# Kernel optimization log

Measured on AMD Instinct MI355X. Metric: run time of the kernel, lower is better.

Reference implementation:

```python
import jax, jax.numpy as jnp
import numpy as np

B, L, DIM = 4, 2048, 1024
EXPAND, D_STATE, D_CONV = 2, 16, 4
D_INNER = EXPAND * DIM          # 2048
DT_RANK = DIM // 16             # 64
MLP_HID = 4 * DIM


def setup_inputs() -> dict:
    key = jax.random.key(0)
    ks = jax.random.split(key, 20)
    s = 0.02
    inp = {
        "hidden_states": jax.random.normal(ks[0], (B, L, DIM), jnp.float32),
        "cond": jax.random.normal(ks[1], (B, DIM), jnp.float32),
        # norm (LayerNorm with affine)
        "norm_w": jnp.ones((DIM,), jnp.float32),
        "norm_b": jnp.zeros((DIM,), jnp.float32),
        # adaLN: Linear(dim, 6*dim)
        "ada_w": jax.random.normal(ks[2], (6 * DIM, DIM), jnp.float32) * s,
        "ada_b": jnp.zeros((6 * DIM,), jnp.float32),
        # Mamba mixer params
        "in_proj_w": jax.random.normal(ks[3], (2 * D_INNER, DIM), jnp.float32) * s,
        "conv_w": jax.random.normal(ks[4], (D_INNER, 1, D_CONV), jnp.float32) * s,
        "conv_b": jnp.zeros((D_INNER,), jnp.float32),
        "x_proj_w": jax.random.normal(ks[5], (DT_RANK + 2 * D_STATE, D_INNER), jnp.float32) * s,
        "dt_proj_w": jax.random.normal(ks[6], (D_INNER, DT_RANK), jnp.float32) * s,
        "dt_proj_b": jax.random.uniform(ks[7], (D_INNER,), jnp.float32, -4.0, -2.0),
        "A_log": jnp.log(jnp.broadcast_to(jnp.arange(1, D_STATE + 1, dtype=jnp.float32), (D_INNER, D_STATE))),
        "Dp": jnp.ones((D_INNER,), jnp.float32),
        "out_proj_w": jax.random.normal(ks[8], (DIM, D_INNER), jnp.float32) * s,
        # MLP
        "fc1_w": jax.random.normal(ks[9], (MLP_HID, DIM), jnp.float32) * s,
        "fc1_b": jnp.zeros((MLP_HID,), jnp.float32),
        "fc2_w": jax.random.normal(ks[10], (DIM, MLP_HID), jnp.float32) * s,
        "fc2_b": jnp.zeros((DIM,), jnp.float32),
    }
    return inp


def _layernorm(x, w, b, eps):
    mu = jnp.mean(x, axis=-1, keepdims=True)
    var = jnp.mean(jnp.square(x - mu), axis=-1, keepdims=True)
    y = (x - mu) * jax.lax.rsqrt(var + eps)
    return y * w + b if w is not None else y


def _modulate(x, shift, scale):
    # x: [B,L,D]; shift/scale: [B,D]
    return x * (1.0 + scale[:, None, :]) + shift[:, None, :]


def _mamba(x_in, in_proj_w, conv_w, conv_b, x_proj_w, dt_proj_w, dt_proj_b, A_log, Dp, out_proj_w):
    # x_in: [B,L,DIM]
    xz = jnp.einsum("bld,ed->ble", x_in, in_proj_w)        # [B,L,2*Di]
    x, z = jnp.split(xz, 2, axis=-1)                        # each [B,L,Di]
    # causal depthwise conv over L
    x_ncl = jnp.transpose(x, (0, 2, 1))                     # [B,Di,L]
    x_ncl = jax.lax.conv_general_dilated(
        x_ncl, conv_w, window_strides=(1,), padding=[(D_CONV - 1, 0)],
        feature_group_count=D_INNER, dimension_numbers=("NCH", "OIH", "NCH"))
    x = jnp.transpose(x_ncl, (0, 2, 1)) + conv_b            # [B,L,Di]
    x = jax.nn.silu(x)
    x_dbl = jnp.einsum("bld,ed->ble", x, x_proj_w)          # [B,L,dt_rank+2*N]
    dt, Bm, Cm = jnp.split(x_dbl, [DT_RANK, DT_RANK + D_STATE], axis=-1)
    dt = jax.nn.softplus(jnp.einsum("blr,dr->bld", dt, dt_proj_w) + dt_proj_b)  # [B,L,Di]
    A = -jnp.exp(A_log)                                     # [Di,N]

    def step(h, inps):
        dt_t, B_t, C_t, x_t = inps                          # [B,Di],[B,N],[B,N],[B,Di]
        dA = jnp.exp(dt_t[..., None] * A)                   # [B,Di,N]
        dBx = (dt_t * x_t)[..., None] * B_t[:, None, :]     # [B,Di,N]
        h = h * dA + dBx
        y = jnp.einsum("bdn,bn->bd", h, C_t)
        return h, y

    h0 = jnp.zeros((x.shape[0], D_INNER, D_STATE), x.dtype)
    xs = (jnp.transpose(dt, (1, 0, 2)), jnp.transpose(Bm, (1, 0, 2)),
          jnp.transpose(Cm, (1, 0, 2)), jnp.transpose(x, (1, 0, 2)))
    _, ys = jax.lax.scan(step, h0, xs)                      # [L,B,Di]
    y = jnp.transpose(ys, (1, 0, 2)) + x * Dp               # [B,L,Di]
    y = y * jax.nn.silu(z)
    return jnp.einsum("bld,od->blo", y, out_proj_w)         # [B,L,DIM]


def reference(hidden_states, cond, norm_w, norm_b, ada_w, ada_b, in_proj_w, conv_w,
              conv_b, x_proj_w, dt_proj_w, dt_proj_b, A_log, Dp, out_proj_w,
              fc1_w, fc1_b, fc2_w, fc2_b):
    residual = hidden_states                                # residual=None path
    hs = _layernorm(residual, norm_w, norm_b, 1e-5)
    mods = jax.nn.silu(cond) @ ada_w.T + ada_b              # [B,6*DIM]
    shift_msa, scale_msa, gate_msa, shift_mlp, scale_mlp, gate_mlp = jnp.split(mods, 6, axis=1)
    hs = gate_msa[:, None, :] * _mamba(_modulate(hs, shift_msa, scale_msa),
                                       in_proj_w, conv_w, conv_b, x_proj_w,
                                       dt_proj_w, dt_proj_b, A_log, Dp, out_proj_w)
    h2 = _modulate(_layernorm(hs, None, None, 1e-6), shift_mlp, scale_mlp)
    h2 = jax.nn.gelu(h2 @ fc1_w.T + fc1_b, approximate=True) @ fc2_w.T + fc2_b
    hs = hs + gate_mlp[:, None, :] * h2
    return (hs, residual)
```

## Files before the change

### kernel.cpp

```cpp
#include <hip/hip_runtime.h>
#include <hip/hip_bf16.h>


typedef unsigned short ushort_t;
typedef __attribute__((ext_vector_type(8))) short short8;
typedef __attribute__((ext_vector_type(4))) float floatx4;
typedef __attribute__((ext_vector_type(4))) unsigned short ushort4v;

#define DEVI __device__ __forceinline__

DEVI float b2f(ushort_t u) { union { unsigned int i; float f; } v; v.i = ((unsigned int)u) << 16; return v.f; }
DEVI ushort_t f2b(float f) {
    union { float f; unsigned int i; } v; v.f = f;
    unsigned int r = v.i + 0x7fffu + ((v.i >> 16) & 1u);
    return (ushort_t)(r >> 16);
}
DEVI float sigmoidf_(float x) { return 1.f / (1.f + __expf(-x)); }
DEVI float siluf_(float x) { return x * sigmoidf_(x); }
DEVI float softplusf_(float x) { return (x > 20.f) ? x : log1pf(__expf(x)); }
DEVI float gelu_tanh_(float x) {
    float c = 0.7978845608028654f * (x + 0.044715f * x * x * x);
    return 0.5f * x * (1.f + tanhf(c));
}
DEVI void async16(ushort_t* lds, const ushort_t* g) {
    __builtin_amdgcn_global_load_lds((const __attribute__((address_space(1))) void*)g,
                                     (__attribute__((address_space(3))) void*)lds,
                                     16, 0, 0);
}

DEVI void remap_tile(int bid, int Mt, int Nt, int& mt, int& nt) {
    const int nwg = Mt * Nt;
    const int cpx = nwg >> 3;
    const int v = (bid & 7) * cpx + (bid >> 3);
    if (((Mt & 7) == 0) && ((Nt & 7) == 0)) {
        const int s = v >> 6, w = v & 63;
        const int smt = s % (Mt >> 3), snt = s / (Mt >> 3);
        mt = smt * 8 + (w >> 3);
        nt = snt * 8 + (w & 7);
    } else {
        mt = v % Mt;
        nt = v / Mt;
    }
}

__global__ void detect_kernel(const void* norm_w, int* flag) {
    if (threadIdx.x == 0)
        flag[0] = (((const unsigned int*)norm_w)[0] == 0x3F800000u) ? 1 : 0;
}

__global__ __launch_bounds__(256) void convert_w_kernel(
    const void* __restrict__ src, ushort_t* __restrict__ dst, int n8,
    const int* __restrict__ flag)
{
    int i = blockIdx.x * 256 + threadIdx.x;
    if (i >= n8) return;
    if (*flag) {
        const float4* s = (const float4*)src;
        float4 a = s[2 * i], b = s[2 * i + 1];
        short8 o;
        o[0] = (short)f2b(a.x); o[1] = (short)f2b(a.y);
        o[2] = (short)f2b(a.z); o[3] = (short)f2b(a.w);
        o[4] = (short)f2b(b.x); o[5] = (short)f2b(b.y);
        o[6] = (short)f2b(b.z); o[7] = (short)f2b(b.w);
        ((short8*)dst)[i] = o;
    } else {
        ((short8*)dst)[i] = ((const short8*)src)[i];
    }
}

__global__ __launch_bounds__(256) void canon_bias_kernel(
    const void* __restrict__ src, float* __restrict__ dst, int n,
    const int* __restrict__ flag)
{
    int i = blockIdx.x * 256 + threadIdx.x;
    if (i >= n) return;
    dst[i] = (*flag) ? ((const float*)src)[i] : b2f(((const ushort_t*)src)[i]);
}

__global__ __launch_bounds__(256) void residual_kernel(
    const void* __restrict__ src, void* __restrict__ dst, const int* __restrict__ flag)
{
    size_t i = (size_t)blockIdx.x * 256 + threadIdx.x;
    if (*flag) {
        ((float4*)((float*)dst + 8388608))[i] = ((const float4*)src)[i];
    } else {
        ((ushort4v*)((ushort_t*)dst + 8388608))[i] = ((const ushort4v*)src)[i];
    }
}

__global__ __launch_bounds__(256) void ada_kernel(
    const void* __restrict__ condv, const void* __restrict__ ada_wv,
    const void* __restrict__ ada_bv, float* __restrict__ mods,
    const int* __restrict__ flag)
{
    __shared__ float sc[4096];
    const int tid = threadIdx.x;
    const bool f32 = (*flag != 0);
    if (f32) {
        const float* cf = (const float*)condv;
        for (int i = tid; i < 4096; i += 256) sc[i] = siluf_(cf[i]);
    } else {
        const ushort_t* cb = (const ushort_t*)condv;
        for (int i = tid; i < 4096; i += 256) sc[i] = siluf_(b2f(cb[i]));
    }
    __syncthreads();
    const int j = blockIdx.x * 256 + tid;
    float bb = f32 ? ((const float*)ada_bv)[j] : b2f(((const ushort_t*)ada_bv)[j]);
    float s0 = bb, s1 = bb, s2 = bb, s3 = bb;
    if (f32) {
        const float4* w4 = ((const float4*)ada_wv) + (size_t)j * 256;
        for (int d4 = 0; d4 < 256; d4++) {
            float4 w = w4[d4];
            float wv[4] = {w.x, w.y, w.z, w.w};
#pragma unroll
            for (int e = 0; e < 4; e++) {
                int d = d4 * 4 + e;
                s0 += sc[d] * wv[e];
                s1 += sc[1024 + d] * wv[e];
                s2 += sc[2048 + d] * wv[e];
                s3 += sc[3072 + d] * wv[e];
            }
        }
    } else {
        const ushort_t* wrow = ((const ushort_t*)ada_wv) + (size_t)j * 1024;
        for (int d = 0; d < 1024; d += 8) {
            short8 w8 = *(const short8*)(wrow + d);
#pragma unroll
            for (int e = 0; e < 8; e++) {
                float wv = b2f(((const ushort_t*)&w8)[e]);
                s0 += sc[d + e] * wv;
                s1 += sc[1024 + d + e] * wv;
                s2 += sc[2048 + d + e] * wv;
                s3 += sc[3072 + d + e] * wv;
            }
        }
    }
    mods[0 * 6144 + j] = s0;
    mods[1 * 6144 + j] = s1;
    mods[2 * 6144 + j] = s2;
    mods[3 * 6144 + j] = s3;
}

__global__ __launch_bounds__(256) void ln1_mod_kernel(
    const void* __restrict__ hiddenv, const void* __restrict__ nwv,
    const void* __restrict__ nbv, const float* __restrict__ mods,
    ushort_t* __restrict__ xout, const int* __restrict__ flag)
{
    const int t = blockIdx.x, tid = threadIdx.x;
    const int bb = t >> 11;
    const bool f32 = (*flag != 0);
    float vv[4], s = 0.f, ss = 0.f;
    if (f32) {
        float4 u = ((const float4*)((const float*)hiddenv + (size_t)t * 1024))[tid];
        vv[0] = u.x; vv[1] = u.y; vv[2] = u.z; vv[3] = u.w;
    } else {
        ushort4v u = ((const ushort4v*)((const ushort_t*)hiddenv + (size_t)t * 1024))[tid];
#pragma unroll
        for (int j = 0; j < 4; j++) vv[j] = b2f(u[j]);
    }
#pragma unroll
    for (int j = 0; j < 4; j++) { s += vv[j]; ss += vv[j] * vv[j]; }
#pragma unroll
    for (int off = 32; off > 0; off >>= 1) { s += __shfl_down(s, off); ss += __shfl_down(ss, off); }
    __shared__ float red[8];
    const int wave = tid >> 6, lane = tid & 63;
    if (lane == 0) { red[wave] = s; red[4 + wave] = ss; }
    __syncthreads();
    s = red[0] + red[1] + red[2] + red[3];
    ss = red[4] + red[5] + red[6] + red[7];
    const float mu = s * (1.f / 1024.f);
    const float var = ss * (1.f / 1024.f) - mu * mu;
    const float rstd = rsqrtf(var + 1e-5f);
    const float* mrow = mods + (size_t)bb * 6144;
    ushort4v o;
#pragma unroll
    for (int j = 0; j < 4; j++) {
        int d = tid * 4 + j;
        float w = f32 ? ((const float*)nwv)[d] : b2f(((const ushort_t*)nwv)[d]);
        float b = f32 ? ((const float*)nbv)[d] : b2f(((const ushort_t*)nbv)[d]);
        float y = (vv[j] - mu) * rstd * w + b;
        y = y * (1.f + mrow[1024 + d]) + mrow[d];
        o[j] = f2b(y);
    }
    ((ushort4v*)(xout + (size_t)t * 1024))[tid] = o;
}

__global__ __launch_bounds__(256) void ln2_mod_kernel(
    const ushort_t* __restrict__ hs, const float* __restrict__ mods,
    ushort_t* __restrict__ xout)
{
    const int t = blockIdx.x, tid = threadIdx.x;
    const int bb = t >> 11;
    ushort4v u = ((const ushort4v*)(hs + (size_t)t * 1024))[tid];
    float vv[4], s = 0.f, ss = 0.f;
#pragma unroll
    for (int j = 0; j < 4; j++) { vv[j] = b2f(u[j]); s += vv[j]; ss += vv[j] * vv[j]; }
#pragma unroll
    for (int off = 32; off > 0; off >>= 1) { s += __shfl_down(s, off); ss += __shfl_down(ss, off); }
    __shared__ float red[8];
    const int wave = tid >> 6, lane = tid & 63;
    if (lane == 0) { red[wave] = s; red[4 + wave] = ss; }
    __syncthreads();
    s = red[0] + red[1] + red[2] + red[3];
    ss = red[4] + red[5] + red[6] + red[7];
    const float mu = s * (1.f / 1024.f);
    const float var = ss * (1.f / 1024.f) - mu * mu;
    const float rstd = rsqrtf(var + 1e-6f);
    const float* mrow = mods + (size_t)bb * 6144;
    ushort4v o;
#pragma unroll
    for (int j = 0; j < 4; j++) {
        int d = tid * 4 + j;
        float y = (vv[j] - mu) * rstd;
        y = y * (1.f + mrow[4096 + d]) + mrow[3072 + d];
        o[j] = f2b(y);
    }
    ((ushort4v*)(xout + (size_t)t * 1024))[tid] = o;
}

__global__ __launch_bounds__(256) void conv_silu_kernel(
    const ushort_t* __restrict__ xb, const void* __restrict__ cwv,
    const void* __restrict__ cbv, ushort_t* __restrict__ xc,
    const int* __restrict__ flag)
{
    const int t = blockIdx.x;
    const int l = t & 2047;
    const int c0 = threadIdx.x * 8;
    const bool f32 = (*flag != 0);
    float acc[8];
    float wlf[32];
    if (f32) {
        const float* cbf = (const float*)cbv;
#pragma unroll
        for (int j = 0; j < 8; j++) acc[j] = cbf[c0 + j];
        const float4* cw4 = (const float4*)((const float*)cwv + (size_t)c0 * 4);
#pragma unroll
        for (int q = 0; q < 8; q++) {
            float4 w = cw4[q];
            wlf[q * 4 + 0] = w.x; wlf[q * 4 + 1] = w.y;
            wlf[q * 4 + 2] = w.z; wlf[q * 4 + 3] = w.w;
        }
    } else {
        const ushort_t* cbb = (const ushort_t*)cbv;
#pragma unroll
        for (int j = 0; j < 8; j++) acc[j] = b2f(cbb[c0 + j]);
        const ushort_t* cwb = (const ushort_t*)cwv + (size_t)c0 * 4;
#pragma unroll
        for (int q = 0; q < 32; q++) wlf[q] = b2f(cwb[q]);
    }
#pragma unroll
    for (int k = 0; k < 4; k++) {
        int tl = l + k - 3;
        if (tl < 0) continue;
        short8 xv = *(const short8*)(xb + (size_t)(t + k - 3) * 2048 + c0);
#pragma unroll
        for (int j = 0; j < 8; j++)
            acc[j] += b2f(((const ushort_t*)&xv)[j]) * wlf[j * 4 + k];
    }
    short8 o;
#pragma unroll
    for (int j = 0; j < 8; j++) ((ushort_t*)&o)[j] = f2b(siluf_(acc[j]));
    *(short8*)(xc + (size_t)t * 2048 + c0) = o;
}

__global__ __launch_bounds__(256) void scan_phase1(
    const ushort_t* __restrict__ dtb, const ushort_t* __restrict__ xcv,
    const ushort_t* __restrict__ xdbl, const void* __restrict__ A_logv,
    ushort_t* __restrict__ Hloc, ushort_t* __restrict__ Pst,
    const int* __restrict__ flag)
{
    const int blk = blockIdx.x;
    const int dblk = blk & 7;
    const int c = (blk >> 3) & 31;
    const int b = blk >> 8;
    const int d = dblk * 256 + threadIdx.x;
    const bool f32 = (*flag != 0);
    float Av[16];
#pragma unroll
    for (int n = 0; n < 16; n++) {
        float al = f32 ? ((const float*)A_logv)[(size_t)d * 16 + n]
                       : b2f(((const ushort_t*)A_logv)[(size_t)d * 16 + n]);
        Av[n] = -__expf(al);
    }
    float h[16], Pa[16];
#pragma unroll
    for (int n = 0; n < 16; n++) { h[n] = 0.f; Pa[n] = 1.f; }
    const int t0 = c * 64;
    size_t tb = ((size_t)b * 2048 + t0) * 2048 + d;
    float dtv = b2f(dtb[tb]);
    float xv  = b2f(xcv[tb]);
    for (int tt = 0; tt < 64; ++tt) {
        float dtn = b2f(dtb[tb + 2048]);
        float xn  = b2f(xcv[tb + 2048]);
        const ushort_t* bp = xdbl + ((size_t)b * 2048 + t0 + tt) * 96 + 64;
        short8 B8a = *(const short8*)bp;
        short8 B8b = *(const short8*)(bp + 8);
        float dtx = dtv * xv;
#pragma unroll
        for (int n = 0; n < 8; n++) {
            float dA = __expf(dtv * Av[n]);
            h[n] = h[n] * dA + dtx * b2f(((const ushort_t*)&B8a)[n]);
            Pa[n] *= dA;
        }
#pragma unroll
        for (int n = 8; n < 16; n++) {
            float dA = __expf(dtv * Av[n]);
            h[n] = h[n] * dA + dtx * b2f(((const ushort_t*)&B8b)[n - 8]);
            Pa[n] *= dA;
        }
        dtv = dtn; xv = xn; tb += 2048;
    }
    const size_t o = (((size_t)c * 4 + b) * 16) * 2048 + d;
#pragma unroll
    for (int n = 0; n < 16; n++) {
        Hloc[o + (size_t)n * 2048] = f2b(h[n]);
        Pst [o + (size_t)n * 2048] = f2b(Pa[n]);
    }
}

__global__ __launch_bounds__(256) void scan_phase2(
    const ushort_t* __restrict__ Hloc, const ushort_t* __restrict__ Pst,
    float* __restrict__ Hin)
{
    const int gi = blockIdx.x * 256 + threadIdx.x;
    const int d = gi & 2047;
    const int n = (gi >> 11) & 15;
    const int b = gi >> 15;
    float h = 0.f;
    const size_t o0 = ((size_t)b * 16 + n) * 2048 + d;
    for (int c = 0; c < 32; ++c) {
        const size_t o = o0 + (size_t)c * (4 * 16 * 2048);
        Hin[o] = h;
        h = b2f(Hloc[o]) + b2f(Pst[o]) * h;
    }
}

__global__ __launch_bounds__(256) void scan_phase3(
    const ushort_t* __restrict__ dtb, ushort_t* __restrict__ xc,
    const ushort_t* __restrict__ xdbl, const ushort_t* __restrict__ zbuf,
    const void* __restrict__ A_logv, const void* __restrict__ Dpv,
    const float* __restrict__ Hin, const int* __restrict__ flag)
{
    const int blk = blockIdx.x;
    const int dblk = blk & 7;
    const int c = (blk >> 3) & 31;
    const int b = blk >> 8;
    const int d = dblk * 256 + threadIdx.x;
    const bool f32 = (*flag != 0);
    float Av[16];
#pragma unroll
    for (int n = 0; n < 16; n++) {
        float al = f32 ? ((const float*)A_logv)[(size_t)d * 16 + n]
                       : b2f(((const ushort_t*)A_logv)[(size_t)d * 16 + n]);
        Av[n] = -__expf(al);
    }
    const float Dv = f32 ? ((const float*)Dpv)[d] : b2f(((const ushort_t*)Dpv)[d]);
    float h[16];
    {
        const size_t o = (((size_t)c * 4 + b) * 16) * 2048 + d;
#pragma unroll
        for (int n = 0; n < 16; n++) h[n] = Hin[o + (size_t)n * 2048];
    }
    const int t0 = c * 64;
    size_t tb = ((size_t)b * 2048 + t0) * 2048 + d;
    float dtv = b2f(dtb[tb]);
    float xv  = b2f(xc[tb]);
    float zv  = b2f(zbuf[tb]);
    for (int tt = 0; tt < 64; ++tt) {
        float dtn = b2f(dtb[tb + 2048]);
        float xn  = b2f(xc[tb + 2048]);
        float zn  = b2f(zbuf[tb + 2048]);
        const ushort_t* bp = xdbl + ((size_t)b * 2048 + t0 + tt) * 96 + 64;
        short8 B8a = *(const short8*)bp;
        short8 B8b = *(const short8*)(bp + 8);
        short8 C8a = *(const short8*)(bp + 16);
        short8 C8b = *(const short8*)(bp + 24);
        float dtx = dtv * xv;
        float y = 0.f;
#pragma unroll
        for (int n = 0; n < 8; n++) {
            float dA = __expf(dtv * Av[n]);
            h[n] = h[n] * dA + dtx * b2f(((const ushort_t*)&B8a)[n]);
            y += h[n] * b2f(((const ushort_t*)&C8a)[n]);
        }
#pragma unroll
        for (int n = 8; n < 16; n++) {
            float dA = __expf(dtv * Av[n]);
            h[n] = h[n] * dA + dtx * b2f(((const ushort_t*)&B8b)[n - 8]);
            y += h[n] * b2f(((const ushort_t*)&C8b)[n - 8]);
        }
        float yo = (y + xv * Dv) * siluf_(zv);
        xc[tb] = f2b(yo);
        dtv = dtn; xv = xn; zv = zn; tb += 2048;
    }
}

template <int EPI>
DEVI void epi_store(int row, int col, float v,
                    void* C0, void* C1, int ldc,
                    const float* bias, const float* mods,
                    const ushort_t* hs, int fl)
{
    if constexpr (EPI == 0) {
        if (col < 2048)
            ((ushort_t*)C0)[(size_t)row * 2048 + col] = f2b(v);
        else
            ((ushort_t*)C1)[(size_t)row * 2048 + (col - 2048)] = f2b(v);
    } else if constexpr (EPI == 1) {
        ((ushort_t*)C0)[(size_t)row * ldc + col] = f2b(v);
    } else if constexpr (EPI == 2) {
        v += bias[col];
        ((ushort_t*)C0)[(size_t)row * ldc + col] = f2b(softplusf_(v));
    } else if constexpr (EPI == 3) {
        const int bb = row >> 11;
        v *= mods[(size_t)bb * 6144 + 2048 + col];
        ((ushort_t*)C0)[(size_t)row * ldc + col] = f2b(v);
    } else if constexpr (EPI == 4) {
        v += bias[col];
        ((ushort_t*)C0)[(size_t)row * ldc + col] = f2b(gelu_tanh_(v));
    } else if constexpr (EPI == 5) {
        v += bias[col];
        const int bb = row >> 11;
        float o = b2f(hs[(size_t)row * 1024 + col]) + mods[(size_t)bb * 6144 + 5120 + col] * v;
        if (fl)
            ((float*)C0)[(size_t)row * ldc + col] = o;
        else
            ((ushort_t*)C0)[(size_t)row * ldc + col] = f2b(o);
    }
}

#define KLOOP_PIPE(NT)                                               \
    stage(0, 0);                                                     \
    {                                                                \
        int cur = 0;                                                 \
        for (int kt = 0; kt < (NT); kt++) {                          \
            if (kt + 1 < (NT)) {                                     \
                stage(cur ^ 1, kt + 1);                              \
                asm volatile("s_waitcnt vmcnt(8)" ::: "memory");     \
            } else {                                                 \
                asm volatile("s_waitcnt vmcnt(0)" ::: "memory");     \
            }                                                        \
            __builtin_amdgcn_sched_barrier(0);                       \
            __builtin_amdgcn_s_barrier();                            \
            __builtin_amdgcn_sched_barrier(0);                       \
            __builtin_amdgcn_s_setprio(1);                           \
            compute(cur);                                            \
            __builtin_amdgcn_s_setprio(0);                           \
            __builtin_amdgcn_sched_barrier(0);                       \
            __builtin_amdgcn_s_barrier();                            \
            __builtin_amdgcn_sched_barrier(0);                       \
            cur ^= 1;                                                \
        }                                                            \
    }

template <int EPI>
__global__ __launch_bounds__(256) void gemm_bt(
    const ushort_t* __restrict__ A, int lda,
    const ushort_t* __restrict__ W,
    int M, int N, int K,
    void* __restrict__ C0, void* __restrict__ C1, int ldc,
    const float* __restrict__ bias,
    const float* __restrict__ mods,
    const ushort_t* __restrict__ hs,
    const int* __restrict__ flag)
{
    __shared__ __align__(16) ushort_t sA[2][128 * 64];
    __shared__ __align__(16) ushort_t sB[2][128 * 64];
    const int tid = threadIdx.x;
    const int wave = tid >> 6, lane = tid & 63;
    int mt, nt;
    remap_tile(blockIdx.x, M >> 7, (N + 127) >> 7, mt, nt);
    const int m0 = mt << 7, n0 = nt << 7;
    const int wr = wave >> 1, wc = wave & 1;
    const int r = tid >> 3, c8 = tid & 7;
    const int rs7 = r & 7;
    int fl = 0;
    if constexpr (EPI == 5) fl = *flag;

    floatx4 acc[4][4];
#pragma unroll
    for (int m = 0; m < 4; m++)
#pragma unroll
        for (int nn = 0; nn < 4; nn++) acc[m][nn] = floatx4{0.f, 0.f, 0.f, 0.f};

    auto stage = [&](int buf, int kt) {
        const int kb = kt << 6;
#pragma unroll
        for (int i = 0; i < 4; i++) {
            const int row = i * 32 + r;
            async16(&sA[buf][(size_t)row * 64 + c8 * 8],
                    A + (size_t)(m0 + row) * lda + kb + ((c8 ^ rs7) << 3));
            int rB = n0 + row; if (rB >= N) rB = N - 1;
            async16(&sB[buf][(size_t)row * 64 + c8 * 8],
                    W + (size_t)rB * K + kb + ((c8 ^ rs7) << 3));
        }
    };
    auto compute = [&](int buf) {
#pragma unroll
        for (int kk = 0; kk < 2; kk++) {
            const int sw = ((kk * 4 + (lane >> 4)) ^ (lane & 7)) << 3;
            short8 bfr[4];
#pragma unroll
            for (int nn = 0; nn < 4; nn++)
                bfr[nn] = *(const short8*)&sB[buf][(size_t)(wc * 64 + nn * 16 + (lane & 15)) * 64 + sw];
#pragma unroll
            for (int m = 0; m < 4; m++) {
                short8 af = *(const short8*)&sA[buf][(size_t)(wr * 64 + m * 16 + (lane & 15)) * 64 + sw];
#pragma unroll
                for (int nn = 0; nn < 4; nn++)
                    acc[m][nn] = __builtin_amdgcn_mfma_f32_16x16x32_bf16(af, bfr[nn], acc[m][nn], 0, 0, 0);
            }
        }
    };

    const int NT = K >> 6;
    KLOOP_PIPE(NT)

    const int erow = wr * 64 + ((lane >> 4) << 2);
    const int ecol = wc * 64 + (lane & 15);
#pragma unroll
    for (int m = 0; m < 4; m++)
#pragma unroll
        for (int nn = 0; nn < 4; nn++) {
            const int col = n0 + ecol + nn * 16;
            if (col >= N) continue;
#pragma unroll
            for (int rr = 0; rr < 4; rr++)
                epi_store<EPI>(m0 + erow + m * 16 + rr, col, acc[m][nn][rr],
                               C0, C1, ldc, bias, mods, hs, fl);
        }
}

template <int EPI>
__global__ __launch_bounds__(512) void gemm256(
    const ushort_t* __restrict__ A, int lda,
    const ushort_t* __restrict__ W,
    int M, int N, int K,
    void* __restrict__ C0, void* __restrict__ C1, int ldc,
    const float* __restrict__ bias,
    const float* __restrict__ mods,
    const ushort_t* __restrict__ hs,
    const int* __restrict__ flag)
{
    __shared__ __align__(16) ushort_t sA[2][256 * 64];
    __shared__ __align__(16) ushort_t sB[2][256 * 64];
    const int tid = threadIdx.x;
    const int wave = tid >> 6, lane = tid & 63;
    int mt, nt;
    remap_tile(blockIdx.x, M >> 8, N >> 8, mt, nt);
    const int m0 = mt << 8, n0 = nt << 8;
    const int wr = wave >> 2, wc = wave & 3;
    const int r = tid >> 3, c8 = tid & 7;
    const int rs7 = r & 7;
    int fl = 0;
    if constexpr (EPI == 5) fl = *flag;

    floatx4 acc[8][4];
#pragma unroll
    for (int m = 0; m < 8; m++)
#pragma unroll
        for (int nn = 0; nn < 4; nn++) acc[m][nn] = floatx4{0.f, 0.f, 0.f, 0.f};

    auto stage = [&](int buf, int kt) {
        const int kb = kt << 6;
#pragma unroll
        for (int i = 0; i < 4; i++) {
            const int row = i * 64 + r;
            async16(&sA[buf][(size_t)row * 64 + c8 * 8],
                    A + (size_t)(m0 + row) * lda + kb + ((c8 ^ rs7) << 3));
            async16(&sB[buf][(size_t)row * 64 + c8 * 8],
                    W + (size_t)(n0 + row) * K + kb + ((c8 ^ rs7) << 3));
        }
    };
    auto compute = [&](int buf) {
#pragma unroll
        for (int kk = 0; kk < 2; kk++) {
            const int sw = ((kk * 4 + (lane >> 4)) ^ (lane & 7)) << 3;
            short8 bfr[4];
#pragma unroll
            for (int nn = 0; nn < 4; nn++)
                bfr[nn] = *(const short8*)&sB[buf][(size_t)(wc * 64 + nn * 16 + (lane & 15)) * 64 + sw];
#pragma unroll
            for (int m = 0; m < 8; m++) {
                short8 af = *(const short8*)&sA[buf][(size_t)(wr * 128 + m * 16 + (lane & 15)) * 64 + sw];
#pragma unroll
                for (int nn = 0; nn < 4; nn++)
                    acc[m][nn] = __builtin_amdgcn_mfma_f32_16x16x32_bf16(af, bfr[nn], acc[m][nn], 0, 0, 0);
            }
        }
    };

    const int NT = K >> 6;
    KLOOP_PIPE(NT)

    const int erow = wr * 128 + ((lane >> 4) << 2);
    const int ecol = wc * 64 + (lane & 15);
#pragma unroll
    for (int m = 0; m < 8; m++)
#pragma unroll
        for (int nn = 0; nn < 4; nn++) {
            const int col = n0 + ecol + nn * 16;
            if (col >= N) continue;
#pragma unroll
            for (int rr = 0; rr < 4; rr++)
                epi_store<EPI>(m0 + erow + m * 16 + rr, col, acc[m][nn][rr],
                               C0, C1, ldc, bias, mods, hs, fl);
        }
}

extern "C" void kernel_launch(void* const* d_in, const int* in_sizes, int n_in,
                              void* d_out, int out_size, void* d_ws, size_t ws_size,
                              hipStream_t stream)
{
    const void* hidden   = d_in[0];
    const void* cond     = d_in[1];
    const void* norm_w   = d_in[2];
    const void* norm_b   = d_in[3];
    const void* ada_w    = d_in[4];
    const void* ada_b    = d_in[5];
    const void* in_proj  = d_in[6];
    const void* conv_w   = d_in[7];
    const void* conv_b   = d_in[8];
    const void* x_proj   = d_in[9];
    const void* dt_w     = d_in[10];
    const void* dt_b     = d_in[11];
    const void* A_log    = d_in[12];
    const void* Dp       = d_in[13];
    const void* out_proj = d_in[14];
    const void* fc1_w    = d_in[15];
    const void* fc1_b    = d_in[16];
    const void* fc2_w    = d_in[17];
    const void* fc2_b    = d_in[18];

    constexpr size_t OFF_FLAG  = 0;
    constexpr size_t OFF_MODS  = 256;
    constexpr size_t OFF_DTB_F = 131072;
    constexpr size_t OFF_FC1B  = 139264;
    constexpr size_t OFF_FC2B  = 155648;
    constexpr size_t OFF_WIN   = 262144;
    constexpr size_t OFF_WXP   = 8650752;
    constexpr size_t OFF_WDT   = 9043968;
    constexpr size_t OFF_WOUT  = 9306112;
    constexpr size_t OFF_WFC1  = 13500416;
    constexpr size_t OFF_WFC2  = 21889024;
    constexpr size_t OFF_XBUF  = 30277632;
    constexpr size_t OFF_ZBUF  = 63832064;
    constexpr size_t OFF_XCONV = 97386496;
    constexpr size_t OFF_XIN   = 130940928;
    constexpr size_t OFF_XDBL  = 147718144;
    constexpr size_t OFF_HS    = 149291008;
    constexpr size_t WS_NEED   = 166068224;
    if (ws_size < WS_NEED) return;

    char* ws = (char*)d_ws;
    int*      flag   = (int*)(ws + OFF_FLAG);
    float*    mods   = (float*)(ws + OFF_MODS);
    float*    dtb_f  = (float*)(ws + OFF_DTB_F);
    float*    fc1b_f = (float*)(ws + OFF_FC1B);
    float*    fc2b_f = (float*)(ws + OFF_FC2B);
    ushort_t* w_in   = (ushort_t*)(ws + OFF_WIN);
    ushort_t* w_xp   = (ushort_t*)(ws + OFF_WXP);
    ushort_t* w_dt   = (ushort_t*)(ws + OFF_WDT);
    ushort_t* w_out  = (ushort_t*)(ws + OFF_WOUT);
    ushort_t* w_fc1  = (ushort_t*)(ws + OFF_WFC1);
    ushort_t* w_fc2  = (ushort_t*)(ws + OFF_WFC2);
    ushort_t* xbuf   = (ushort_t*)(ws + OFF_XBUF);
    ushort_t* zbuf   = (ushort_t*)(ws + OFF_ZBUF);
    ushort_t* x_conv = (ushort_t*)(ws + OFF_XCONV);
    ushort_t* x_in   = (ushort_t*)(ws + OFF_XIN);
    ushort_t* x_dbl  = (ushort_t*)(ws + OFF_XDBL);
    ushort_t* hsb    = (ushort_t*)(ws + OFF_HS);
    ushort_t* dtb    = xbuf;
    ushort_t* h1     = xbuf;
    ushort_t* h2in   = x_in;
    ushort_t* Hloc   = (ushort_t*)(ws + OFF_XIN);
    ushort_t* Pst    = (ushort_t*)(ws + OFF_XIN + 8388608);
    float*    Hin    = (float*)(ws + OFF_HS);

    detect_kernel<<<1, 64, 0, stream>>>(norm_w, flag);

    convert_w_kernel<<<2048, 256, 0, stream>>>(in_proj, w_in, 524288, flag);
    convert_w_kernel<<<96, 256, 0, stream>>>(x_proj, w_xp, 24576, flag);
    convert_w_kernel<<<64, 256, 0, stream>>>(dt_w, w_dt, 16384, flag);
    convert_w_kernel<<<1024, 256, 0, stream>>>(out_proj, w_out, 262144, flag);
    convert_w_kernel<<<2048, 256, 0, stream>>>(fc1_w, w_fc1, 524288, flag);
    convert_w_kernel<<<2048, 256, 0, stream>>>(fc2_w, w_fc2, 524288, flag);
    canon_bias_kernel<<<8, 256, 0, stream>>>(dt_b, dtb_f, 2048, flag);
    canon_bias_kernel<<<16, 256, 0, stream>>>(fc1_b, fc1b_f, 4096, flag);
    canon_bias_kernel<<<4, 256, 0, stream>>>(fc2_b, fc2b_f, 1024, flag);

    residual_kernel<<<8192, 256, 0, stream>>>(hidden, d_out, flag);

    ada_kernel<<<24, 256, 0, stream>>>(cond, ada_w, ada_b, mods, flag);
    ln1_mod_kernel<<<8192, 256, 0, stream>>>(hidden, norm_w, norm_b, mods, x_in, flag);
    gemm256<0><<<32 * 16, 512, 0, stream>>>(x_in, 1024, w_in, 8192, 4096, 1024,
                                            xbuf, zbuf, 2048, nullptr, nullptr, nullptr, flag);
    conv_silu_kernel<<<8192, 256, 0, stream>>>(xbuf, conv_w, conv_b, x_conv, flag);
    gemm_bt<1><<<64 * 1, 256, 0, stream>>>(x_conv, 2048, w_xp, 8192, 96, 2048,
                                           x_dbl, nullptr, 96, nullptr, nullptr, nullptr, flag);
    gemm_bt<2><<<64 * 16, 256, 0, stream>>>(x_dbl, 96, w_dt, 8192, 2048, 64,
                                            dtb, nullptr, 2048, dtb_f, nullptr, nullptr, flag);
    scan_phase1<<<1024, 256, 0, stream>>>(dtb, x_conv, x_dbl, A_log, Hloc, Pst, flag);
    scan_phase2<<<512, 256, 0, stream>>>(Hloc, Pst, Hin);
    scan_phase3<<<1024, 256, 0, stream>>>(dtb, x_conv, x_dbl, zbuf, A_log, Dp, Hin, flag);
    gemm_bt<3><<<64 * 8, 256, 0, stream>>>(x_conv, 2048, w_out, 8192, 1024, 2048,
                                           hsb, nullptr, 1024, nullptr, mods, nullptr, flag);
    ln2_mod_kernel<<<8192, 256, 0, stream>>>(hsb, mods, h2in);
    gemm256<4><<<32 * 16, 512, 0, stream>>>(h2in, 1024, w_fc1, 8192, 4096, 1024,
                                            h1, nullptr, 4096, fc1b_f, nullptr, nullptr, flag);
    gemm_bt<5><<<64 * 8, 256, 0, stream>>>(h1, 4096, w_fc2, 8192, 1024, 4096,
                                           d_out, nullptr, 1024, fc2b_f, mods, hsb, flag);
}
```

Before: 775.6 us.

## Merge prep kernels, split-K x_proj GEMM, phase-pipelined 256 GEMM with finer LDS staging

All weight and bias conversions now run in one launch, and the dtype flag is computed inline from norm_w, so the detect kernel is gone. The residual copy is folded into the first layernorm kernel. The skinny x_proj GEMM (N=96) becomes a 4-way split-K into fp32 partials followed by a reduce kernel, raising its block count from 64 to 256. The 256-tile GEMM is restructured into four K-phases per tile with barriers, prefetch interleaved per phase, setprio around the MFMAs and a new LDS layout. This adds more barriers per K step and an extra partial-sum pass through memory.

New measurement: 757.0 us. -2.4%, faster.

```diff
diff --git a/kernel.cpp b/kernel.cpp
--- a/kernel.cpp
+++ b/kernel.cpp
@@ -15,6 +15,7 @@
     unsigned int r = v.i + 0x7fffu + ((v.i >> 16) & 1u);
     return (ushort_t)(r >> 16);
 }
+DEVI bool is_f32(const void* nw) { return ((const unsigned int*)nw)[0] == 0x3F800000u; }
 DEVI float sigmoidf_(float x) { return 1.f / (1.f + __expf(-x)); }
 DEVI float siluf_(float x) { return x * sigmoidf_(x); }
 DEVI float softplusf_(float x) { return (x > 20.f) ? x : log1pf(__expf(x)); }
@@ -43,59 +44,61 @@
     }
 }
 
-__global__ void detect_kernel(const void* norm_w, int* flag) {
-    if (threadIdx.x == 0)
-        flag[0] = (((const unsigned int*)norm_w)[0] == 0x3F800000u) ? 1 : 0;
-}
-
-__global__ __launch_bounds__(256) void convert_w_kernel(
-    const void* __restrict__ src, ushort_t* __restrict__ dst, int n8,
-    const int* __restrict__ flag)
-{
-    int i = blockIdx.x * 256 + threadIdx.x;
+__global__ __launch_bounds__(256) void convert_all_kernel(
+    const void* __restrict__ in_proj, const void* __restrict__ x_proj,
+    const void* __restrict__ dt_w, const void* __restrict__ out_proj,
+    const void* __restrict__ fc1_w, const void* __restrict__ fc2_w,
+    const void* __restrict__ dt_b, const void* __restrict__ fc1_b,
+    const void* __restrict__ fc2_b,
+    ushort_t* __restrict__ w_in, ushort_t* __restrict__ w_xp,
+    ushort_t* __restrict__ w_dt, ushort_t* __restrict__ w_out,
+    ushort_t* __restrict__ w_fc1, ushort_t* __restrict__ w_fc2,
+    float* __restrict__ dtb_f, float* __restrict__ fc1b_f,
+    float* __restrict__ fc2b_f, const void* __restrict__ nw)
+{
+    const bool f32 = is_f32(nw);
+    int b = blockIdx.x;
+    const void* src; ushort_t* dst; int n8;
+    if (b < 2048)      { src = in_proj;  dst = w_in;  n8 = 524288; }
+    else if (b < 2144) { src = x_proj;   dst = w_xp;  n8 = 24576;  b -= 2048; }
+    else if (b < 2208) { src = dt_w;     dst = w_dt;  n8 = 16384;  b -= 2144; }
+    else if (b < 3232) { src = out_proj; dst = w_out; n8 = 262144; b -= 2208; }
+    else if (b < 5280) { src = fc1_w;    dst = w_fc1; n8 = 524288; b -= 3232; }
+    else if (b < 7328) { src = fc2_w;    dst = w_fc2; n8 = 524288; b -= 5280; }
+    else {
+        b -= 7328;
+        const void* bs; float* bd; int n;
+        if (b < 8)       { bs = dt_b;  bd = dtb_f;  n = 2048; }
+        else if (b < 24) { bs = fc1_b; bd = fc1b_f; n = 4096; b -= 8; }
+        else             { bs = fc2_b; bd = fc2b_f; n = 1024; b -= 24; }
+        int i = b * 256 + threadIdx.x;
+        if (i < n) bd[i] = f32 ? ((const float*)bs)[i] : b2f(((const ushort_t*)bs)[i]);
+        return;
+    }
+    int i = b * 256 + threadIdx.x;
     if (i >= n8) return;
-    if (*flag) {
+    if (f32) {
         const float4* s = (const float4*)src;
-        float4 a = s[2 * i], b = s[2 * i + 1];
+        float4 a = s[2 * i], c = s[2 * i + 1];
         short8 o;
         o[0] = (short)f2b(a.x); o[1] = (short)f2b(a.y);
         o[2] = (short)f2b(a.z); o[3] = (short)f2b(a.w);
-        o[4] = (short)f2b(b.x); o[5] = (short)f2b(b.y);
-        o[6] = (short)f2b(b.z); o[7] = (short)f2b(b.w);
+        o[4] = (short)f2b(c.x); o[5] = (short)f2b(c.y);
+        o[6] = (short)f2b(c.z); o[7] = (short)f2b(c.w);
         ((short8*)dst)[i] = o;
     } else {
         ((short8*)dst)[i] = ((const short8*)src)[i];
     }
 }
 
-__global__ __launch_bounds__(256) void canon_bias_kernel(
-    const void* __restrict__ src, float* __restrict__ dst, int n,
-    const int* __restrict__ flag)
-{
-    int i = blockIdx.x * 256 + threadIdx.x;
-    if (i >= n) return;
-    dst[i] = (*flag) ? ((const float*)src)[i] : b2f(((const ushort_t*)src)[i]);
-}
-
-__global__ __launch_bounds__(256) void residual_kernel(
-    const void* __restrict__ src, void* __restrict__ dst, const int* __restrict__ flag)
-{
-    size_t i = (size_t)blockIdx.x * 256 + threadIdx.x;
-    if (*flag) {
-        ((float4*)((float*)dst + 8388608))[i] = ((const float4*)src)[i];
-    } else {
-        ((ushort4v*)((ushort_t*)dst + 8388608))[i] = ((const ushort4v*)src)[i];
-    }
-}
-
 __global__ __launch_bounds__(256) void ada_kernel(
     const void* __restrict__ condv, const void* __restrict__ ada_wv,
     const void* __restrict__ ada_bv, float* __restrict__ mods,
-    const int* __restrict__ flag)
+    const void* __restrict__ nw)
 {
     __shared__ float sc[4096];
     const int tid = threadIdx.x;
-    const bool f32 = (*flag != 0);
+    const bool f32 = is_f32(nw);
     if (f32) {
         const float* cf = (const float*)condv;
         for (int i = tid; i < 4096; i += 256) sc[i] = siluf_(cf[i]);
@@ -141,22 +144,24 @@
     mods[3 * 6144 + j] = s3;
 }
 
-__global__ __launch_bounds__(256) void ln1_mod_kernel(
+__global__ __launch_bounds__(256) void ln1_res_kernel(
     const void* __restrict__ hiddenv, const void* __restrict__ nwv,
     const void* __restrict__ nbv, const float* __restrict__ mods,
-    ushort_t* __restrict__ xout, const int* __restrict__ flag)
+    ushort_t* __restrict__ xout, void* __restrict__ dout)
 {
     const int t = blockIdx.x, tid = threadIdx.x;
     const int bb = t >> 11;
-    const bool f32 = (*flag != 0);
+    const bool f32 = is_f32(nwv);
     float vv[4], s = 0.f, ss = 0.f;
     if (f32) {
         float4 u = ((const float4*)((const float*)hiddenv + (size_t)t * 1024))[tid];
         vv[0] = u.x; vv[1] = u.y; vv[2] = u.z; vv[3] = u.w;
+        ((float4*)((float*)dout + 8388608))[(size_t)t * 256 + tid] = u;
     } else {
         ushort4v u = ((const ushort4v*)((const ushort_t*)hiddenv + (size_t)t * 1024))[tid];
 #pragma unroll
         for (int j = 0; j < 4; j++) vv[j] = b2f(u[j]);
+        ((ushort4v*)((ushort_t*)dout + 8388608))[(size_t)t * 256 + tid] = u;
     }
 #pragma unroll
     for (int j = 0; j < 4; j++) { s += vv[j]; ss += vv[j] * vv[j]; }
@@ -221,12 +226,12 @@
 __global__ __launch_bounds__(256) void conv_silu_kernel(
     const ushort_t* __restrict__ xb, const void* __restrict__ cwv,
     const void* __restrict__ cbv, ushort_t* __restrict__ xc,
-    const int* __restrict__ flag)
+    const void* __restrict__ nw)
 {
     const int t = blockIdx.x;
     const int l = t & 2047;
     const int c0 = threadIdx.x * 8;
-    const bool f32 = (*flag != 0);
+    const bool f32 = is_f32(nw);
     float acc[8];
     float wlf[32];
     if (f32) {
@@ -267,14 +272,14 @@
     const ushort_t* __restrict__ dtb, const ushort_t* __restrict__ xcv,
     const ushort_t* __restrict__ xdbl, const void* __restrict__ A_logv,
     ushort_t* __restrict__ Hloc, ushort_t* __restrict__ Pst,
-    const int* __restrict__ flag)
+    const void* __restrict__ nw)
 {
     const int blk = blockIdx.x;
     const int dblk = blk & 7;
     const int c = (blk >> 3) & 31;
     const int b = blk >> 8;
     const int d = dblk * 256 + threadIdx.x;
-    const bool f32 = (*flag != 0);
+    const bool f32 = is_f32(nw);
     float Av[16];
 #pragma unroll
     for (int n = 0; n < 16; n++) {
@@ -339,14 +344,14 @@
     const ushort_t* __restrict__ dtb, ushort_t* __restrict__ xc,
     const ushort_t* __restrict__ xdbl, const ushort_t* __restrict__ zbuf,
     const void* __restrict__ A_logv, const void* __restrict__ Dpv,
-    const float* __restrict__ Hin, const int* __restrict__ flag)
+    const float* __restrict__ Hin, const void* __restrict__ nw)
 {
     const int blk = blockIdx.x;
     const int dblk = blk & 7;
     const int c = (blk >> 3) & 31;
     const int b = blk >> 8;
     const int d = dblk * 256 + threadIdx.x;
-    const bool f32 = (*flag != 0);
+    const bool f32 = is_f32(nw);
     float Av[16];
 #pragma unroll
     for (int n = 0; n < 16; n++) {
@@ -426,6 +431,8 @@
             ((float*)C0)[(size_t)row * ldc + col] = o;
         else
             ((ushort_t*)C0)[(size_t)row * ldc + col] = f2b(o);
+    } else if constexpr (EPI == 6) {
+        ((float*)C0)[(size_t)row * ldc + col] = v;
     }
 }
 
@@ -456,26 +463,34 @@
 template <int EPI>
 __global__ __launch_bounds__(256) void gemm_bt(
     const ushort_t* __restrict__ A, int lda,
-    const ushort_t* __restrict__ W,
+    const ushort_t* __restrict__ W, int ldw,
     int M, int N, int K,
     void* __restrict__ C0, void* __restrict__ C1, int ldc,
     const float* __restrict__ bias,
     const float* __restrict__ mods,
     const ushort_t* __restrict__ hs,
-    const int* __restrict__ flag)
+    const void* __restrict__ nwp)
 {
     __shared__ __align__(16) ushort_t sA[2][128 * 64];
     __shared__ __align__(16) ushort_t sB[2][128 * 64];
     const int tid = threadIdx.x;
     const int wave = tid >> 6, lane = tid & 63;
     int mt, nt;
-    remap_tile(blockIdx.x, M >> 7, (N + 127) >> 7, mt, nt);
+    if constexpr (EPI == 6) {
+        mt = blockIdx.x & 63; nt = 0;
+        const int kc = blockIdx.x >> 6;
+        A += (size_t)kc * 512;
+        W += (size_t)kc * 512;
+        C0 = (float*)C0 + (size_t)kc * 8192 * 96;
+    } else {
+        remap_tile(blockIdx.x, M >> 7, (N + 127) >> 7, mt, nt);
+    }
     const int m0 = mt << 7, n0 = nt << 7;
     const int wr = wave >> 1, wc = wave & 1;
     const int r = tid >> 3, c8 = tid & 7;
     const int rs7 = r & 7;
     int fl = 0;
-    if constexpr (EPI == 5) fl = *flag;
+    if constexpr (EPI == 5) fl = is_f32(nwp) ? 1 : 0;
 
     floatx4 acc[4][4];
 #pragma unroll
@@ -492,7 +507,7 @@
                     A + (size_t)(m0 + row) * lda + kb + ((c8 ^ rs7) << 3));
             int rB = n0 + row; if (rB >= N) rB = N - 1;
             async16(&sB[buf][(size_t)row * 64 + c8 * 8],
-                    W + (size_t)rB * K + kb + ((c8 ^ rs7) << 3));
+                    W + (size_t)rB * ldw + kb + ((c8 ^ rs7) << 3));
         }
     };
     auto compute = [&](int buf) {
@@ -534,26 +549,27 @@
 template <int EPI>
 __global__ __launch_bounds__(512) void gemm256(
     const ushort_t* __restrict__ A, int lda,
-    const ushort_t* __restrict__ W,
+    const ushort_t* __restrict__ W, int ldw,
     int M, int N, int K,
     void* __restrict__ C0, void* __restrict__ C1, int ldc,
     const float* __restrict__ bias,
     const float* __restrict__ mods,
     const ushort_t* __restrict__ hs,
-    const int* __restrict__ flag)
-{
-    __shared__ __align__(16) ushort_t sA[2][256 * 64];
-    __shared__ __align__(16) ushort_t sB[2][256 * 64];
+    const void* __restrict__ nwp)
+{
+    __shared__ __align__(16) ushort_t sA[2][4][256 * 16];
+    __shared__ __align__(16) ushort_t sB[2][4][256 * 16];
     const int tid = threadIdx.x;
     const int wave = tid >> 6, lane = tid & 63;
+    const int l15 = lane & 15, j8 = lane >> 4;
     int mt, nt;
     remap_tile(blockIdx.x, M >> 8, N >> 8, mt, nt);
     const int m0 = mt << 8, n0 = nt << 8;
     const int wr = wave >> 2, wc = wave & 3;
-    const int r = tid >> 3, c8 = tid & 7;
-    const int rs7 = r & 7;
+    const int srow = tid >> 1, scs = tid & 1;
+    const int ssrc = scs ^ ((srow >> 2) & 1);
     int fl = 0;
-    if constexpr (EPI == 5) fl = *flag;
+    if constexpr (EPI == 5) fl = is_f32(nwp) ? 1 : 0;
 
     floatx4 acc[8][4];
 #pragma unroll
@@ -561,40 +577,67 @@
 #pragma unroll
         for (int nn = 0; nn < 4; nn++) acc[m][nn] = floatx4{0.f, 0.f, 0.f, 0.f};
 
-    auto stage = [&](int buf, int kt) {
-        const int kb = kt << 6;
-#pragma unroll
-        for (int i = 0; i < 4; i++) {
-            const int row = i * 64 + r;
-            async16(&sA[buf][(size_t)row * 64 + c8 * 8],
-                    A + (size_t)(m0 + row) * lda + kb + ((c8 ^ rs7) << 3));
-            async16(&sB[buf][(size_t)row * 64 + c8 * 8],
-                    W + (size_t)(n0 + row) * K + kb + ((c8 ^ rs7) << 3));
-        }
+    auto stage = [&](int buf, int kt, int p) {
+        const int kb = (kt << 6) + (p << 4);
+        async16(&sA[buf][p][srow * 16 + scs * 8],
+                A + (size_t)(m0 + srow) * lda + kb + ssrc * 8);
+        async16(&sB[buf][p][srow * 16 + scs * 8],
+                W + (size_t)(n0 + srow) * ldw + kb + ssrc * 8);
     };
-    auto compute = [&](int buf) {
-#pragma unroll
-        for (int kk = 0; kk < 2; kk++) {
-            const int sw = ((kk * 4 + (lane >> 4)) ^ (lane & 7)) << 3;
-            short8 bfr[4];
-#pragma unroll
-            for (int nn = 0; nn < 4; nn++)
-                bfr[nn] = *(const short8*)&sB[buf][(size_t)(wc * 64 + nn * 16 + (lane & 15)) * 64 + sw];
-#pragma unroll
-            for (int m = 0; m < 8; m++) {
-                short8 af = *(const short8*)&sA[buf][(size_t)(wr * 128 + m * 16 + (lane & 15)) * 64 + sw];
-#pragma unroll
-                for (int nn = 0; nn < 4; nn++)
-                    acc[m][nn] = __builtin_amdgcn_mfma_f32_16x16x32_bf16(af, bfr[nn], acc[m][nn], 0, 0, 0);
-            }
-        }
-    };
+
+#define G256_PHASE(P, MLO, KK)                                                  \
+    {                                                                           \
+        if (pre) {                                                              \
+            stage(cur ^ 1, kt + 1, P);                                          \
+            asm volatile("s_waitcnt vmcnt(4)" ::: "memory");                    \
+        } else if (P == 2) {                                                    \
+            asm volatile("s_waitcnt vmcnt(0)" ::: "memory");                    \
+        }                                                                       \
+        __builtin_amdgcn_sched_barrier(0);                                      \
+        __builtin_amdgcn_s_barrier();                                           \
+        __builtin_amdgcn_sched_barrier(0);                                      \
+        short8 bfr[4], af[4];                                                   \
+        _Pragma("unroll")                                                       \
+        for (int nn = 0; nn < 4; nn++) {                                        \
+            const int row = wc * 64 + nn * 16 + l15;                            \
+            bfr[nn] = *(const short8*)&sB[cur][(KK) * 2 + (j8 >> 1)]            \
+                          [row * 16 + (((j8 & 1) ^ ((row >> 2) & 1)) << 3)];    \
+        }                                                                       \
+        _Pragma("unroll")                                                       \
+        for (int i = 0; i < 4; i++) {                                           \
+            const int row = wr * 128 + ((MLO) + i) * 16 + l15;                  \
+            af[i] = *(const short8*)&sA[cur][(KK) * 2 + (j8 >> 1)]              \
+                        [row * 16 + (((j8 & 1) ^ ((row >> 2) & 1)) << 3)];      \
+        }                                                                       \
+        __builtin_amdgcn_s_setprio(1);                                          \
+        _Pragma("unroll")                                                       \
+        for (int i = 0; i < 4; i++)                                             \
+            _Pragma("unroll")                                                   \
+            for (int nn = 0; nn < 4; nn++)                                      \
+                acc[(MLO) + i][nn] = __builtin_amdgcn_mfma_f32_16x16x32_bf16(   \
+                    af[i], bfr[nn], acc[(MLO) + i][nn], 0, 0, 0);               \
+        __builtin_amdgcn_s_setprio(0);                                          \
+    }
 
     const int NT = K >> 6;
-    KLOOP_PIPE(NT)
-
-    const int erow = wr * 128 + ((lane >> 4) << 2);
-    const int ecol = wc * 64 + (lane & 15);
+#pragma unroll
+    for (int p = 0; p < 4; p++) stage(0, 0, p);
+    int cur = 0;
+    for (int kt = 0; kt < NT; kt++) {
+        const bool pre = (kt + 1 < NT);
+        G256_PHASE(0, 0, 0)
+        G256_PHASE(1, 4, 0)
+        G256_PHASE(2, 0, 1)
+        G256_PHASE(3, 4, 1)
+        __builtin_amdgcn_sched_barrier(0);
+        __builtin_amdgcn_s_barrier();
+        __builtin_amdgcn_sched_barrier(0);
+        cur ^= 1;
+    }
+#undef G256_PHASE
+
+    const int erow = wr * 128 + (j8 << 2);
+    const int ecol = wc * 64 + l15;
 #pragma unroll
     for (int m = 0; m < 8; m++)
 #pragma unroll
@@ -606,6 +649,14 @@
                 epi_store<EPI>(m0 + erow + m * 16 + rr, col, acc[m][nn][rr],
                                C0, C1, ldc, bias, mods, hs, fl);
         }
+}
+
+__global__ __launch_bounds__(256) void xp_reduce_kernel(
+    const float* __restrict__ part, ushort_t* __restrict__ x_dbl)
+{
+    const int i = blockIdx.x * 256 + threadIdx.x;
+    float s = part[i] + part[i + 786432] + part[i + 2 * 786432] + part[i + 3 * 786432];
+    x_dbl[i] = f2b(s);
 }
 
 extern "C" void kernel_launch(void* const* d_in, const int* in_sizes, int n_in,
@@ -632,7 +683,6 @@
     const void* fc2_w    = d_in[17];
     const void* fc2_b    = d_in[18];
 
-    constexpr size_t OFF_FLAG  = 0;
     constexpr size_t OFF_MODS  = 256;
     constexpr size_t OFF_DTB_F = 131072;
     constexpr size_t OFF_FC1B  = 139264;
@@ -653,7 +703,6 @@
     if (ws_size < WS_NEED) return;
 
     char* ws = (char*)d_ws;
-    int*      flag   = (int*)(ws + OFF_FLAG);
     float*    mods   = (float*)(ws + OFF_MODS);
     float*    dtb_f  = (float*)(ws + OFF_DTB_F);
     float*    fc1b_f = (float*)(ws + OFF_FC1B);
@@ -673,41 +722,33 @@
     ushort_t* dtb    = xbuf;
     ushort_t* h1     = xbuf;
     ushort_t* h2in   = x_in;
+    float*    xp_part= (float*)(ws + OFF_XIN);
     ushort_t* Hloc   = (ushort_t*)(ws + OFF_XIN);
     ushort_t* Pst    = (ushort_t*)(ws + OFF_XIN + 8388608);
     float*    Hin    = (float*)(ws + OFF_HS);
 
-    detect_kernel<<<1, 64, 0, stream>>>(norm_w, flag);
-
-    convert_w_kernel<<<2048, 256, 0, stream>>>(in_proj, w_in, 524288, flag);
-    convert_w_kernel<<<96, 256, 0, stream>>>(x_proj, w_xp, 24576, flag);
-    convert_w_kernel<<<64, 256, 0, stream>>>(dt_w, w_dt, 16384, flag);
-    convert_w_kernel<<<1024, 256, 0, stream>>>(out_proj, w_out, 262144, flag);
-    convert_w_kernel<<<2048, 256, 0, stream>>>(fc1_w, w_fc1, 524288, flag);
-    convert_w_kernel<<<2048, 256, 0, stream>>>(fc2_w, w_fc2, 524288, flag);
-    canon_bias_kernel<<<8, 256, 0, stream>>>(dt_b, dtb_f, 2048, flag);
-    canon_bias_kernel<<<16, 256, 0, stream>>>(fc1_b, fc1b_f, 4096, flag);
-    canon_bias_kernel<<<4, 256, 0, stream>>>(fc2_b, fc2b_f, 1024, flag);
-
-    residual_kernel<<<8192, 256, 0, stream>>>(hidden, d_out, flag);
-
-    ada_kernel<<<24, 256, 0, stream>>>(cond, ada_w, ada_b, mods, flag);
-    ln1_mod_kernel<<<8192, 256, 0, stream>>>(hidden, norm_w, norm_b, mods, x_in, flag);
-    gemm256<0><<<32 * 16, 512, 0, stream>>>(x_in, 1024, w_in, 8192, 4096, 1024,
-                                            xbuf, zbuf, 2048, nullptr, nullptr, nullptr, flag);
-    conv_silu_kernel<<<8192, 256, 0, stream>>>(xbuf, conv_w, conv_b, x_conv, flag);
-    gemm_bt<1><<<64 * 1, 256, 0, stream>>>(x_conv, 2048, w_xp, 8192, 96, 2048,
-                                           x_dbl, nullptr, 96, nullptr, nullptr, nullptr, flag);
-    gemm_bt<2><<<64 * 16, 256, 0, stream>>>(x_dbl, 96, w_dt, 8192, 2048, 64,
-                                            dtb, nullptr, 2048, dtb_f, nullptr, nullptr, flag);
-    scan_phase1<<<1024, 256, 0, stream>>>(dtb, x_conv, x_dbl, A_log, Hloc, Pst, flag);
+    convert_all_kernel<<<7356, 256, 0, stream>>>(
+        in_proj, x_proj, dt_w, out_proj, fc1_w, fc2_w, dt_b, fc1_b, fc2_b,
+        w_in, w_xp, w_dt, w_out, w_fc1, w_fc2, dtb_f, fc1b_f, fc2b_f, norm_w);
+
+    ada_kernel<<<24, 256, 0, stream>>>(cond, ada_w, ada_b, mods, norm_w);
+    ln1_res_kernel<<<8192, 256, 0, stream>>>(hidden, norm_w, norm_b, mods, x_in, d_out);
+    gemm256<0><<<512, 512, 0, stream>>>(x_in, 1024, w_in, 1024, 8192, 4096, 1024,
+                                        xbuf, zbuf, 2048, nullptr, nullptr, nullptr, nullptr);
+    conv_silu_kernel<<<8192, 256, 0, stream>>>(xbuf, conv_w, conv_b, x_conv, norm_w);
+    gemm_bt<6><<<256, 256, 0, stream>>>(x_conv, 2048, w_xp, 2048, 8192, 96, 512,
+                                        xp_part, nullptr, 96, nullptr, nullptr, nullptr, nullptr);
+    xp_reduce_kernel<<<3072, 256, 0, stream>>>(xp_part, x_dbl);
+    gemm_bt<2><<<1024, 256, 0, stream>>>(x_dbl, 96, w_dt, 64, 8192, 2048, 64,
+                                         dtb, nullptr, 2048, dtb_f, nullptr, nullptr, nullptr);
+    scan_phase1<<<1024, 256, 0, stream>>>(dtb, x_conv, x_dbl, A_log, Hloc, Pst, norm_w);
     scan_phase2<<<512, 256, 0, stream>>>(Hloc, Pst, Hin);
-    scan_phase3<<<1024, 256, 0, stream>>>(dtb, x_conv, x_dbl, zbuf, A_log, Dp, Hin, flag);
-    gemm_bt<3><<<64 * 8, 256, 0, stream>>>(x_conv, 2048, w_out, 8192, 1024, 2048,
-                                           hsb, nullptr, 1024, nullptr, mods, nullptr, flag);
+    scan_phase3<<<1024, 256, 0, stream>>>(dtb, x_conv, x_dbl, zbuf, A_log, Dp, Hin, norm_w);
+    gemm_bt<3><<<512, 256, 0, stream>>>(x_conv, 2048, w_out, 2048, 8192, 1024, 2048,
+                                        hsb, nullptr, 1024, nullptr, mods, nullptr, nullptr);
     ln2_mod_kernel<<<8192, 256, 0, stream>>>(hsb, mods, h2in);
-    gemm256<4><<<32 * 16, 512, 0, stream>>>(h2in, 1024, w_fc1, 8192, 4096, 1024,
-                                            h1, nullptr, 4096, fc1b_f, nullptr, nullptr, flag);
-    gemm_bt<5><<<64 * 8, 256, 0, stream>>>(h1, 4096, w_fc2, 8192, 1024, 4096,
-                                           d_out, nullptr, 1024, fc2b_f, mods, hsb, flag);
-}
+    gemm256<4><<<512, 512, 0, stream>>>(h2in, 1024, w_fc1, 1024, 8192, 4096, 1024,
+                                        h1, nullptr, 4096, fc1b_f, nullptr, nullptr, nullptr);
+    gemm_bt<5><<<512, 256, 0, stream>>>(h1, 4096, w_fc2, 4096, 8192, 1024, 4096,
+                                        d_out, nullptr, 1024, fc2b_f, mods, hsb, norm_w);
+}
```
